# Kernel tuning notes

Measured on AMD Instinct MI355X. Metric: run time of the kernel, lower is better.

Reference implementation:

```python
import jax, jax.numpy as jnp
import numpy as np

EPS = 1e-5

def layer_norm(x, g, b):
    mu = jnp.mean(x, axis=-1, keepdims=True)
    var = jnp.var(x, axis=-1, keepdims=True)
    return (x - mu) * jax.lax.rsqrt(var + EPS) * g + b

def rel_shift(x):
    # x: [N, H, T1, T2] with T2 = 2*T1 - 1 -> [N, H, T1, T1]
    N, H, T1, T2 = x.shape
    zp = jnp.zeros((N, H, T1, 1), dtype=x.dtype)
    xp = jnp.concatenate([zp, x], axis=-1).reshape(N, H, T2 + 1, T1)
    x = xp[:, :, 1:, :].reshape(N, H, T1, T2)
    return x[:, :, :, : T2 // 2 + 1]

def setup_inputs() -> dict:
    B, T, D, Hh = 8, 1024, 512, 8
    dk = D // Hh
    P = 2 * T - 1
    key = jax.random.key(0)
    ks = jax.random.split(key, 12)
    s = 0.02
    return {
        "q": jax.random.normal(ks[0], (B, T, D), jnp.float32),
        "k": jax.random.normal(ks[1], (B, T, D), jnp.float32),
        "v": jax.random.normal(ks[2], (B, T, D), jnp.float32),
        "pos_emb": jax.random.normal(ks[3], (1, P, D), jnp.float32),
        "mask": jnp.ones((B, T, T), jnp.int32),
        "ln_q_g": jnp.ones((D,), jnp.float32), "ln_q_b": jnp.zeros((D,), jnp.float32),
        "ln_k_g": jnp.ones((D,), jnp.float32), "ln_k_b": jnp.zeros((D,), jnp.float32),
        "ln_v_g": jnp.ones((D,), jnp.float32), "ln_v_b": jnp.zeros((D,), jnp.float32),
        "w_q": jax.random.normal(ks[4], (D, D), jnp.float32) * s,   # [out, in]
        "w_k": jax.random.normal(ks[5], (D, D), jnp.float32) * s,
        "w_v": jax.random.normal(ks[6], (D, D), jnp.float32) * s,
        "w_pos": jax.random.normal(ks[7], (D, D), jnp.float32) * s,
        "w_fc": jax.random.normal(ks[8], (D, D), jnp.float32) * s,
        "pos_bias_u": jax.random.normal(ks[9], (Hh, dk), jnp.float32) * s,
        "pos_bias_v": jax.random.normal(ks[10], (Hh, dk), jnp.float32) * s,
    }

def reference(q, k, v, pos_emb, mask, ln_q_g, ln_q_b, ln_k_g, ln_k_b, ln_v_g, ln_v_b,
              w_q, w_k, w_v, w_pos, w_fc, pos_bias_u, pos_bias_v):
    B, T, D = q.shape
    H, dk = pos_bias_u.shape
    scale = 1.0 / np.sqrt(dk).astype(np.float32)
    residual = q
    qn = layer_norm(q, ln_q_g, ln_q_b)
    kn = layer_norm(k, ln_k_g, ln_k_b)
    vn = layer_norm(v, ln_v_g, ln_v_b)
    # projections (torch Linear: x @ W^T), reshape to [B, H, T, dk]
    qh = (qn @ w_q.T).reshape(B, T, H, dk)                      # [B, T, H, dk]
    kh = (kn @ w_k.T).reshape(B, T, H, dk).transpose(0, 2, 1, 3)  # [B, H, T, dk]
    vh = (vn @ w_v.T).reshape(B, T, H, dk).transpose(0, 2, 1, 3)
    p = (pos_emb @ w_pos.T).reshape(pos_emb.shape[0], -1, H, dk).transpose(0, 2, 1, 3)  # [1, H, P, dk]
    q_u = (qh + pos_bias_u).transpose(0, 2, 1, 3)  # [B, H, T, dk]
    q_v = (qh + pos_bias_v).transpose(0, 2, 1, 3)
    matrix_ac = jnp.einsum('bhqd,bhkd->bhqk', q_u, kh)          # [B, H, T, T]
    matrix_bd = jnp.einsum('bhqd,nhpd->bhqp', q_v, p)           # [B, H, T, 2T-1]
    matrix_bd = rel_shift(matrix_bd)                             # [B, H, T, T]
    scores = (matrix_ac + matrix_bd) * scale
    m = (mask[:, None, :, :] == 0)                               # [B, 1, T, T]
    scores = jnp.where(m, -jnp.inf, scores)
    attn = jax.nn.softmax(scores, axis=-1)
    attn = jnp.where(m, 0.0, attn)
    out = jnp.einsum('bhqk,bhkd->bhqd', attn, vh)                # [B, H, T, dk]
    out = out.transpose(0, 2, 1, 3).reshape(B, T, H * dk)
    out = out @ w_fc.T + residual
    return out, attn
```

## Files before the change

### kernel.cpp

```cpp
#include <hip/hip_runtime.h>

constexpr int cT  = 1024;
constexpr int cD  = 512;
constexpr int cDK = 64;
constexpr int cP  = 2047;
constexpr int PBS = 1040;

typedef __attribute__((ext_vector_type(8))) short short8;
typedef __attribute__((ext_vector_type(4))) float floatx4;

#define MFMA16(a,b,c) __builtin_amdgcn_mfma_f32_16x16x32_bf16((a),(b),(c),0,0,0)
#define SWZ(i,j) ((j) ^ ((((i) >> 2) & 3) << 3))

__device__ __forceinline__ void bar_lds(){
  asm volatile("s_waitcnt lgkmcnt(0)\n\ts_barrier" ::: "memory");
}

__device__ __forceinline__ unsigned short f2bf(float f){
  union { float f; unsigned int u; } x; x.f = f;
  unsigned int r = x.u + 0x7fffu + ((x.u >> 16) & 1u);
  return (unsigned short)(r >> 16);
}
__device__ __forceinline__ float bf2f(unsigned short h){
  union { unsigned int u; float f; } x; x.u = ((unsigned int)h) << 16;
  return x.f;
}
__device__ __forceinline__ short8 ld8(const unsigned short* p){
  return *(const short8*)p;
}

struct LN3 { const float* x[3]; const float* g[3]; const float* b[3]; unsigned short* y[3]; };
__global__ void __launch_bounds__(256) ln3_kernel(LN3 a)
{
  __shared__ float red[8];
  const int z = blockIdx.y, r = blockIdx.x;
  const float* x = a.x[z]; const float* g = a.g[z]; const float* b = a.b[z];
  unsigned short* y = a.y[z];
  const float2 v = ((const float2*)(x + (size_t)r * cD))[threadIdx.x];
  float s = v.x + v.y, sq = v.x * v.x + v.y * v.y;
  #pragma unroll
  for (int o = 32; o; o >>= 1){ s += __shfl_xor(s, o); sq += __shfl_xor(sq, o); }
  const int w = threadIdx.x >> 6;
  if ((threadIdx.x & 63) == 0){ red[w * 2] = s; red[w * 2 + 1] = sq; }
  __syncthreads();
  s  = red[0] + red[2] + red[4] + red[6];
  sq = red[1] + red[3] + red[5] + red[7];
  const float mu  = s * (1.0f / cD);
  const float var = sq * (1.0f / cD) - mu * mu;
  const float rs  = rsqrtf(var + 1e-5f);
  const int c = threadIdx.x * 2;
  const unsigned int o0 = f2bf((v.x - mu) * rs * g[c]     + b[c]);
  const unsigned int o1 = f2bf((v.y - mu) * rs * g[c + 1] + b[c + 1]);
  ((unsigned int*)(y + (size_t)r * cD))[threadIdx.x] = o0 | (o1 << 16);
}

struct Ptr5 { const float* p[5]; };
__global__ void __launch_bounds__(256) cast5_kernel(Ptr5 s, unsigned short* __restrict__ d){
  const int idx = blockIdx.x * 256 + threadIdx.x;
  const int seg = idx >> 18, off = idx & 262143;
  d[idx] = f2bf(s.p[seg][off]);
}
__global__ void __launch_bounds__(256) cast1_kernel(const float* __restrict__ s,
    unsigned short* __restrict__ d, int n){
  const int idx = blockIdx.x * 256 + threadIdx.x;
  if (idx < n) d[idx] = f2bf(s[idx]);
}

__global__ void __launch_bounds__(256) maskbits_kernel(
    const int* __restrict__ mask, unsigned int* __restrict__ bm)
{
  const int row = blockIdx.x * 4 + (threadIdx.x >> 6);
  const int lane = threadIdx.x & 63;
  #pragma unroll
  for (int ii = 0; ii < 16; ii++){
    const int m = mask[(size_t)row * cT + ii * 64 + lane];
    const unsigned long long bal = __ballot(m != 0);
    if (lane == 0)       bm[row * 32 + ii * 2]     = (unsigned int)bal;
    else if (lane == 32) bm[row * 32 + ii * 2 + 1] = (unsigned int)(bal >> 32);
  }
}

__global__ void __launch_bounds__(256, 4) gemm512_kernel(
    const unsigned short* __restrict__ A0, const unsigned short* __restrict__ W0,
    int M, int mode, float scaleA, unsigned short* __restrict__ outb,
    float* __restrict__ outf, const float* __restrict__ residual)
{
  const int z = blockIdx.z;
  const unsigned short* A = A0 + (size_t)z * 4194304;
  const unsigned short* W = W0 + (size_t)z * 262144;
  unsigned short* outz = outb ? outb + (size_t)z * 4194304 : outb;
  const float sA = (z == 0) ? scaleA : 1.0f;
  const int n0 = blockIdx.x * 128, m0 = blockIdx.y * 128;
  const int wave = threadIdx.x >> 6, lane = threadIdx.x & 63;
  const int wr = wave >> 1, wc = wave & 1;
  const int l15 = lane & 15, lq = lane >> 4;
  const int mb = m0 + wr * 64, nb = n0 + wc * 64;
  floatx4 acc[4][4];
  #pragma unroll
  for (int i = 0; i < 4; i++)
    #pragma unroll
    for (int j = 0; j < 4; j++) acc[i][j] = (floatx4){0.f, 0.f, 0.f, 0.f};
  #pragma unroll 2
  for (int k0 = 0; k0 < 512; k0 += 32){
    short8 af[4], bf[4];
    #pragma unroll
    for (int i = 0; i < 4; i++){
      int row = mb + i * 16 + l15; if (row >= M) row = M - 1;
      af[i] = ld8(A + (size_t)row * 512 + k0 + lq * 8);
      const int col = nb + i * 16 + l15;
      bf[i] = ld8(W + (size_t)col * 512 + k0 + lq * 8);
    }
    #pragma unroll
    for (int i = 0; i < 4; i++)
      #pragma unroll
      for (int j = 0; j < 4; j++)
        acc[i][j] = MFMA16(af[i], bf[j], acc[i][j]);
  }
  #pragma unroll
  for (int i = 0; i < 4; i++){
    #pragma unroll
    for (int j = 0; j < 4; j++){
      #pragma unroll
      for (int r = 0; r < 4; r++){
        const int row = mb + i * 16 + lq * 4 + r;
        const int col = nb + j * 16 + l15;
        if (row >= M) continue;
        const float val = acc[i][j][r] * sA;
        if (mode == 0){
          const int bb = row >> 10, t = row & 1023, h = col >> 6, d = col & 63;
          outz[(((size_t)(bb * 8 + h) * 1024 + t) << 6) + d] = f2bf(val);
        } else if (mode == 1){
          const int h = col >> 6, d = col & 63;
          outz[(((size_t)h * 2047 + row) << 6) + d] = f2bf(val);
        } else {
          const size_t idx = (size_t)row * 512 + col;
          outf[idx] = val + residual[idx];
        }
      }
    }
  }
}

__global__ void __launch_bounds__(256) transpose_v_kernel(
    const unsigned short* __restrict__ vh, unsigned short* __restrict__ vt)
{
  __shared__ unsigned short tile[64][65];
  const int bh = blockIdx.x, t0 = blockIdx.y * 64;
  const unsigned short* src = vh + ((size_t)bh * cT + t0) * cDK;
  #pragma unroll
  for (int i = 0; i < 16; i++){
    const int idx = threadIdx.x + i * 256;
    tile[idx >> 6][idx & 63] = src[idx];
  }
  __syncthreads();
  unsigned short* dst = vt + (size_t)bh * cDK * cT + t0;
  #pragma unroll
  for (int i = 0; i < 16; i++){
    const int idx = threadIdx.x + i * 256;
    const int d = idx >> 6, t = idx & 63;
    dst[(size_t)d * cT + t] = tile[t][d];
  }
}

__global__ void __launch_bounds__(256) dot_bias_kernel(
    const unsigned short* __restrict__ X, const float* __restrict__ bias,
    float* __restrict__ out, int rows, int hdiv, float scale)
{
  const int row = blockIdx.x * 4 + (threadIdx.x >> 6);
  const int lane = threadIdx.x & 63;
  if (row >= rows) return;
  const int h = (row / hdiv) & 7;
  float s = bf2f(X[(size_t)row * 64 + lane]) * bias[h * 64 + lane];
  #pragma unroll
  for (int o = 32; o; o >>= 1) s += __shfl_xor(s, o);
  if (lane == 0) out[row] = s * scale;
}

__global__ void __launch_bounds__(512, 4) attn_kernel(
    const unsigned short* __restrict__ qh, const unsigned short* __restrict__ kh,
    const unsigned short* __restrict__ vt, const unsigned short* __restrict__ pproj,
    const float* __restrict__ ubias, const float* __restrict__ vbias,
    const unsigned int* __restrict__ bm, float* __restrict__ attn_out,
    unsigned short* __restrict__ out_h)
{
  __shared__ float sc[16 * cT];
  unsigned short* pbuf = (unsigned short*)sc;
  const int bh = blockIdx.x, b = bh >> 3, h = bh & 7;
  const int q0 = blockIdx.y * 16;
  const int wave = threadIdx.x >> 6, lane = threadIdx.x & 63;
  const int l15 = lane & 15, lq = lane >> 4;
  const unsigned short* Q  = qh + (size_t)bh * cT * cDK;
  const unsigned short* Kp = kh + (size_t)bh * cT * cDK;
  const unsigned short* Pt = pproj + (size_t)h * cP * cDK;
  const float* ub = ubias + (size_t)bh * cT;
  const float* vb = vbias + (size_t)h * cP;

  const short8 qf0 = ld8(Q + (size_t)(q0 + l15) * cDK + lq * 8);
  const short8 qf1 = ld8(Q + (size_t)(q0 + l15) * cDK + 32 + lq * 8);

  #pragma unroll
  for (int t = 0; t < 8; t++){
    const int jt = wave + t * 8;
    const short8 kf0 = ld8(Kp + (size_t)(jt * 16 + l15) * cDK + lq * 8);
    const short8 kf1 = ld8(Kp + (size_t)(jt * 16 + l15) * cDK + 32 + lq * 8);
    floatx4 acc = (floatx4){0.f, 0.f, 0.f, 0.f};
    acc = MFMA16(qf0, kf0, acc);
    acc = MFMA16(qf1, kf1, acc);
    const int jb = jt * 16 + l15;
    const float ubv = ub[jb];
    #pragma unroll
    for (int r = 0; r < 4; r++){
      const int i = lq * 4 + r;
      sc[i * cT + (jb ^ (lq << 3))] = acc[r] + ubv + vb[jb + (cT - 1) - (q0 + i)];
    }
  }
  bar_lds();

  const int w0 = (cT - 1) - q0 - 15;
  #pragma unroll
  for (int t = 0; t < 8; t++){
    const int ct = wave + t * 8;
    const int c = ct * 16 + l15;
    int prow = w0 + c; if (prow > cP - 1) prow = cP - 1;
    const short8 pf0 = ld8(Pt + (size_t)prow * cDK + lq * 8);
    const short8 pf1 = ld8(Pt + (size_t)prow * cDK + 32 + lq * 8);
    floatx4 acc = (floatx4){0.f, 0.f, 0.f, 0.f};
    acc = MFMA16(qf0, pf0, acc);
    acc = MFMA16(qf1, pf1, acc);
    #pragma unroll
    for (int r = 0; r < 4; r++){
      const int i = lq * 4 + r;
      const int j = c - 15 + i;
      if (j >= 0 && j < cT) sc[i * cT + SWZ(i, j)] += acc[r];
    }
  }
  if (wave == 0){
    const int c = 1024 + l15;
    int prow = w0 + c; if (prow > cP - 1) prow = cP - 1;
    const short8 pf0 = ld8(Pt + (size_t)prow * cDK + lq * 8);
    const short8 pf1 = ld8(Pt + (size_t)prow * cDK + 32 + lq * 8);
    floatx4 acc = (floatx4){0.f, 0.f, 0.f, 0.f};
    acc = MFMA16(qf0, pf0, acc);
    acc = MFMA16(qf1, pf1, acc);
    #pragma unroll
    for (int r = 0; r < 4; r++){
      const int i = lq * 4 + r;
      const int j = c - 15 + i;
      if (j >= 0 && j < cT) sc[i * cT + SWZ(i, j)] += acc[r];
    }
  }
  bar_lds();

  const unsigned short* V = vt + (size_t)bh * cDK * cT;
  const int d0 = (wave & 3) * 16;
  const int kh2 = wave >> 2;
  short8 vfr[8];
  #pragma unroll
  for (int ks = 0; ks < 8; ks++){
    const int j0v = (kh2 * 16 + ks) * 32;
    vfr[ks] = ld8(V + (size_t)(d0 + l15) * cT + j0v + lq * 8);
  }

  for (int p = 0; p < 2; p++){
    const int i = p * 8 + wave;
    const int qrow = q0 + i;
    const unsigned int* bmr = bm + ((size_t)b * cT + qrow) * 32;
    const int xr = ((i >> 2) & 3) << 3;
    float vals[16];
    float mx = -INFINITY;
    #pragma unroll
    for (int ii = 0; ii < 4; ii++){
      const int j0 = lane * 4 + ii * 256;
      const unsigned int mw = bmr[(lane >> 3) + ii * 8] >> (4 * (lane & 7));
      const floatx4 sv = *(const floatx4*)&sc[i * cT + (j0 ^ xr)];
      #pragma unroll
      for (int tt = 0; tt < 4; tt++){
        float s = sv[tt];
        if (((mw >> tt) & 1u) == 0u) s = -INFINITY;
        vals[ii * 4 + tt] = s;
        mx = fmaxf(mx, s);
      }
    }
    #pragma unroll
    for (int o = 32; o; o >>= 1) mx = fmaxf(mx, __shfl_xor(mx, o));
    float sum = 0.f;
    #pragma unroll
    for (int ii = 0; ii < 16; ii++){
      const float e = (vals[ii] == -INFINITY) ? 0.f : __expf(vals[ii] - mx);
      vals[ii] = e; sum += e;
    }
    #pragma unroll
    for (int o = 32; o; o >>= 1) sum += __shfl_xor(sum, o);
    const float ri = sum > 0.f ? 1.f / sum : 0.f;
    bar_lds();
    float* arow = attn_out + ((size_t)bh * cT + qrow) * cT;
    unsigned short* prow_lds = pbuf + (size_t)i * PBS;
    #pragma unroll
    for (int ii = 0; ii < 4; ii++){
      const int j0 = lane * 4 + ii * 256;
      floatx4 pv;
      #pragma unroll
      for (int tt = 0; tt < 4; tt++) pv[tt] = vals[ii * 4 + tt] * ri;
      __builtin_nontemporal_store(pv, (floatx4*)(arow + j0));
      const unsigned int wlo = (unsigned int)f2bf(pv[0]) | ((unsigned int)f2bf(pv[1]) << 16);
      const unsigned int whi = (unsigned int)f2bf(pv[2]) | ((unsigned int)f2bf(pv[3]) << 16);
      *(unsigned long long*)(prow_lds + j0) =
          (unsigned long long)wlo | ((unsigned long long)whi << 32);
    }
  }
  bar_lds();

  floatx4 acc = (floatx4){0.f, 0.f, 0.f, 0.f};
  #pragma unroll
  for (int ks = 0; ks < 8; ks++){
    const int j0 = (kh2 * 16 + ks) * 32;
    const short8 af = ld8(pbuf + l15 * PBS + j0 + lq * 8);
    acc = MFMA16(af, vfr[ks], acc);
  }
  #pragma unroll
  for (int ks = 8; ks < 16; ks++){
    const int j0 = (kh2 * 16 + ks) * 32;
    const short8 vf = ld8(V + (size_t)(d0 + l15) * cT + j0 + lq * 8);
    const short8 af = ld8(pbuf + l15 * PBS + j0 + lq * 8);
    acc = MFMA16(af, vf, acc);
  }
  float* red4 = sc + 10240;
  if (kh2 == 1) *(floatx4*)(red4 + ((wave & 3) * 256 + lane * 4)) = acc;
  bar_lds();
  if (kh2 == 0){
    acc += *(const floatx4*)(red4 + ((wave & 3) * 256 + lane * 4));
    #pragma unroll
    for (int r = 0; r < 4; r++){
      const int i = lq * 4 + r;
      out_h[((size_t)b * cT + q0 + i) * cD + h * cDK + d0 + l15] = f2bf(acc[r]);
    }
  }
}

extern "C" void kernel_launch(void* const* d_in, const int* in_sizes, int n_in,
                              void* d_out, int out_size, void* d_ws, size_t ws_size,
                              hipStream_t stream)
{
  const float* q    = (const float*)d_in[0];
  const float* k    = (const float*)d_in[1];
  const float* v    = (const float*)d_in[2];
  const float* pe   = (const float*)d_in[3];
  const int*   mask = (const int*)d_in[4];
  const float* lnqg = (const float*)d_in[5];
  const float* lnqb = (const float*)d_in[6];
  const float* lnkg = (const float*)d_in[7];
  const float* lnkb = (const float*)d_in[8];
  const float* lnvg = (const float*)d_in[9];
  const float* lnvb = (const float*)d_in[10];
  const float* wq   = (const float*)d_in[11];
  const float* wk   = (const float*)d_in[12];
  const float* wv   = (const float*)d_in[13];
  const float* wpos = (const float*)d_in[14];
  const float* wfc  = (const float*)d_in[15];
  const float* pbu  = (const float*)d_in[16];
  const float* pbv  = (const float*)d_in[17];

  float* out_f  = (float*)d_out;
  float* attn_f = out_f + (size_t)8 * 1024 * 512;

  unsigned char* scr = (unsigned char*)attn_f;
  size_t soff = 0;
  auto salloc = [&](size_t bytes){ void* p = scr + soff; soff += (bytes + 255) & ~(size_t)255; return p; };
  unsigned short* qn   = (unsigned short*)salloc((size_t)8192 * 512 * 2);
  unsigned short* kn   = (unsigned short*)salloc((size_t)8192 * 512 * 2);
  unsigned short* vn   = (unsigned short*)salloc((size_t)8192 * 512 * 2);
  unsigned short* pe_b = (unsigned short*)salloc((size_t)2047 * 512 * 2);
  (void)kn; (void)vn;

  unsigned char* ws = (unsigned char*)d_ws;
  size_t off = 0;
  auto alloc = [&](size_t bytes){ void* p = ws + off; off += (bytes + 255) & ~(size_t)255; return p; };
  unsigned short* w5_b = (unsigned short*)alloc(5 * 512 * 512 * 2);
  unsigned short* qhb  = (unsigned short*)alloc((size_t)8192 * 512 * 2);
  unsigned short* khb  = (unsigned short*)alloc((size_t)8192 * 512 * 2);
  unsigned short* vhb  = (unsigned short*)alloc((size_t)8192 * 512 * 2);
  unsigned short* vtb  = (unsigned short*)alloc((size_t)8192 * 512 * 2);
  unsigned short* ppb  = (unsigned short*)alloc((size_t)8 * 2047 * 64 * 2);
  float*          ub   = (float*)alloc((size_t)8 * 8 * 1024 * 4);
  float*          vbias= (float*)alloc((size_t)8 * 2047 * 4);
  unsigned short* ohb  = (unsigned short*)alloc((size_t)8192 * 512 * 2);
  unsigned int*   bmask= (unsigned int*)alloc((size_t)8192 * 32 * 4);
  (void)ws_size; (void)n_in; (void)in_sizes; (void)out_size;

  Ptr5 c5; c5.p[0] = wq; c5.p[1] = wk; c5.p[2] = wv; c5.p[3] = wpos; c5.p[4] = wfc;
  cast5_kernel<<<5120, 256, 0, stream>>>(c5, w5_b);
  cast1_kernel<<<4094, 256, 0, stream>>>(pe, pe_b, 2047 * 512);
  maskbits_kernel<<<2048, 256, 0, stream>>>(mask, bmask);

  LN3 l3;
  l3.x[0] = q; l3.x[1] = k; l3.x[2] = v;
  l3.g[0] = lnqg; l3.g[1] = lnkg; l3.g[2] = lnvg;
  l3.b[0] = lnqb; l3.b[1] = lnkb; l3.b[2] = lnvb;
  l3.y[0] = qn; l3.y[1] = kn; l3.y[2] = vn;
  ln3_kernel<<<dim3(8192, 3), 256, 0, stream>>>(l3);

  gemm512_kernel<<<dim3(4, 64, 3), 256, 0, stream>>>(qn, w5_b, 8192, 0, 0.125f,
                                                     qhb, nullptr, nullptr);
  gemm512_kernel<<<dim3(4, 16, 1), 256, 0, stream>>>(pe_b, w5_b + 3 * 262144, 2047, 1, 1.0f,
                                                     ppb, nullptr, nullptr);

  transpose_v_kernel<<<dim3(64, 16), 256, 0, stream>>>(vhb, vtb);

  dot_bias_kernel<<<16384, 256, 0, stream>>>(khb, pbu, ub, 65536, 1024, 0.125f);
  dot_bias_kernel<<<4094, 256, 0, stream>>>(ppb, pbv, vbias, 16376, 2047, 0.125f);

  attn_kernel<<<dim3(64, 64), 512, 0, stream>>>(qhb, khb, vtb, ppb, ub, vbias,
                                                bmask, attn_f, ohb);

  gemm512_kernel<<<dim3(4, 64, 1), 256, 0, stream>>>(ohb, w5_b + 4 * 262144, 8192, 2, 1.0f,
                                                     nullptr, out_f, q);
}
```

Measured before the change: 686.5 us.

## Fold pos_bias_u into Q projection, drop ub kernel, prefetch K/P/V fragments

The u-bias term is folded into the Q projection epilogue by adding pos_bias_u to q before scaling. The v-bias dot product then uses (pos_bias_v - pos_bias_u), which removes the per-key ub dot_bias kernel, its buffer, and its per-element reads inside attention. The attention kernel also batches its K and P fragment loads ahead of the MFMAs, hoists the vbias reads, and prefetches the second half of the V fragments before the second softmax pass. The LayerNorm kernel now handles two rows per block with float4 loads. The extra register arrays raise register pressure, which can reduce occupancy of the attention kernel.

```diff
diff --git a/kernel.cpp b/kernel.cpp
--- a/kernel.cpp
+++ b/kernel.cpp
@@ -33,25 +33,33 @@
 __global__ void __launch_bounds__(256) ln3_kernel(LN3 a)
 {
   __shared__ float red[8];
-  const int z = blockIdx.y, r = blockIdx.x;
+  const int z = blockIdx.y;
+  const int half = threadIdx.x >> 7;
+  const int r = blockIdx.x * 2 + half;
+  const int tid = threadIdx.x & 127;
   const float* x = a.x[z]; const float* g = a.g[z]; const float* b = a.b[z];
   unsigned short* y = a.y[z];
-  const float2 v = ((const float2*)(x + (size_t)r * cD))[threadIdx.x];
-  float s = v.x + v.y, sq = v.x * v.x + v.y * v.y;
+  const float4 v = ((const float4*)(x + (size_t)r * cD))[tid];
+  float s  = v.x + v.y + v.z + v.w;
+  float sq = v.x * v.x + v.y * v.y + v.z * v.z + v.w * v.w;
   #pragma unroll
   for (int o = 32; o; o >>= 1){ s += __shfl_xor(s, o); sq += __shfl_xor(sq, o); }
-  const int w = threadIdx.x >> 6;
-  if ((threadIdx.x & 63) == 0){ red[w * 2] = s; red[w * 2 + 1] = sq; }
+  const int w = (threadIdx.x >> 6) & 1;
+  if ((threadIdx.x & 63) == 0){ red[half * 4 + w * 2] = s; red[half * 4 + w * 2 + 1] = sq; }
   __syncthreads();
-  s  = red[0] + red[2] + red[4] + red[6];
-  sq = red[1] + red[3] + red[5] + red[7];
+  s  = red[half * 4]     + red[half * 4 + 2];
+  sq = red[half * 4 + 1] + red[half * 4 + 3];
   const float mu  = s * (1.0f / cD);
   const float var = sq * (1.0f / cD) - mu * mu;
   const float rs  = rsqrtf(var + 1e-5f);
-  const int c = threadIdx.x * 2;
-  const unsigned int o0 = f2bf((v.x - mu) * rs * g[c]     + b[c]);
-  const unsigned int o1 = f2bf((v.y - mu) * rs * g[c + 1] + b[c + 1]);
-  ((unsigned int*)(y + (size_t)r * cD))[threadIdx.x] = o0 | (o1 << 16);
+  const int c = tid * 4;
+  const float4 gv = *(const float4*)(g + c);
+  const float4 bv = *(const float4*)(b + c);
+  const unsigned int o0 = (unsigned int)f2bf((v.x - mu) * rs * gv.x + bv.x)
+                        | ((unsigned int)f2bf((v.y - mu) * rs * gv.y + bv.y) << 16);
+  const unsigned int o1 = (unsigned int)f2bf((v.z - mu) * rs * gv.z + bv.z)
+                        | ((unsigned int)f2bf((v.w - mu) * rs * gv.w + bv.w) << 16);
+  ((uint2*)(y + (size_t)r * cD))[tid] = make_uint2(o0, o1);
 }
 
 struct Ptr5 { const float* p[5]; };
@@ -83,7 +91,8 @@
 __global__ void __launch_bounds__(256, 4) gemm512_kernel(
     const unsigned short* __restrict__ A0, const unsigned short* __restrict__ W0,
     int M, int mode, float scaleA, unsigned short* __restrict__ outb,
-    float* __restrict__ outf, const float* __restrict__ residual)
+    float* __restrict__ outf, const float* __restrict__ residual,
+    const float* __restrict__ addq)
 {
   const int z = blockIdx.z;
   const unsigned short* A = A0 + (size_t)z * 4194304;
@@ -125,7 +134,9 @@
         const int row = mb + i * 16 + lq * 4 + r;
         const int col = nb + j * 16 + l15;
         if (row >= M) continue;
-        const float val = acc[i][j][r] * sA;
+        float val = acc[i][j][r];
+        if (mode == 0 && z == 0 && addq) val += addq[col];
+        val *= sA;
         if (mode == 0){
           const int bb = row >> 10, t = row & 1023, h = col >> 6, d = col & 63;
           outz[(((size_t)(bb * 8 + h) * 1024 + t) << 6) + d] = f2bf(val);
@@ -164,13 +175,16 @@
 
 __global__ void __launch_bounds__(256) dot_bias_kernel(
     const unsigned short* __restrict__ X, const float* __restrict__ bias,
-    float* __restrict__ out, int rows, int hdiv, float scale)
+    const float* __restrict__ bias2, float* __restrict__ out,
+    int rows, int hdiv, float scale)
 {
   const int row = blockIdx.x * 4 + (threadIdx.x >> 6);
   const int lane = threadIdx.x & 63;
   if (row >= rows) return;
   const int h = (row / hdiv) & 7;
-  float s = bf2f(X[(size_t)row * 64 + lane]) * bias[h * 64 + lane];
+  float bv = bias[h * 64 + lane];
+  if (bias2) bv -= bias2[h * 64 + lane];
+  float s = bf2f(X[(size_t)row * 64 + lane]) * bv;
   #pragma unroll
   for (int o = 32; o; o >>= 1) s += __shfl_xor(s, o);
   if (lane == 0) out[row] = s * scale;
@@ -179,9 +193,8 @@
 __global__ void __launch_bounds__(512, 4) attn_kernel(
     const unsigned short* __restrict__ qh, const unsigned short* __restrict__ kh,
     const unsigned short* __restrict__ vt, const unsigned short* __restrict__ pproj,
-    const float* __restrict__ ubias, const float* __restrict__ vbias,
-    const unsigned int* __restrict__ bm, float* __restrict__ attn_out,
-    unsigned short* __restrict__ out_h)
+    const float* __restrict__ vbias, const unsigned int* __restrict__ bm,
+    float* __restrict__ attn_out, unsigned short* __restrict__ out_h)
 {
   __shared__ float sc[16 * cT];
   unsigned short* pbuf = (unsigned short*)sc;
@@ -192,46 +205,59 @@
   const unsigned short* Q  = qh + (size_t)bh * cT * cDK;
   const unsigned short* Kp = kh + (size_t)bh * cT * cDK;
   const unsigned short* Pt = pproj + (size_t)h * cP * cDK;
-  const float* ub = ubias + (size_t)bh * cT;
   const float* vb = vbias + (size_t)h * cP;
 
   const short8 qf0 = ld8(Q + (size_t)(q0 + l15) * cDK + lq * 8);
   const short8 qf1 = ld8(Q + (size_t)(q0 + l15) * cDK + 32 + lq * 8);
 
-  #pragma unroll
-  for (int t = 0; t < 8; t++){
-    const int jt = wave + t * 8;
-    const short8 kf0 = ld8(Kp + (size_t)(jt * 16 + l15) * cDK + lq * 8);
-    const short8 kf1 = ld8(Kp + (size_t)(jt * 16 + l15) * cDK + 32 + lq * 8);
-    floatx4 acc = (floatx4){0.f, 0.f, 0.f, 0.f};
-    acc = MFMA16(qf0, kf0, acc);
-    acc = MFMA16(qf1, kf1, acc);
-    const int jb = jt * 16 + l15;
-    const float ubv = ub[jb];
-    #pragma unroll
-    for (int r = 0; r < 4; r++){
-      const int i = lq * 4 + r;
-      sc[i * cT + (jb ^ (lq << 3))] = acc[r] + ubv + vb[jb + (cT - 1) - (q0 + i)];
+  {
+    short8 k0a[8], k1a[8];
+    #pragma unroll
+    for (int t = 0; t < 8; t++){
+      const int jt = wave + t * 8;
+      k0a[t] = ld8(Kp + (size_t)(jt * 16 + l15) * cDK + lq * 8);
+      k1a[t] = ld8(Kp + (size_t)(jt * 16 + l15) * cDK + 32 + lq * 8);
+    }
+    #pragma unroll
+    for (int t = 0; t < 8; t++){
+      const int jt = wave + t * 8;
+      floatx4 acc = (floatx4){0.f, 0.f, 0.f, 0.f};
+      acc = MFMA16(qf0, k0a[t], acc);
+      acc = MFMA16(qf1, k1a[t], acc);
+      const int jb = jt * 16 + l15;
+      #pragma unroll
+      for (int r = 0; r < 4; r++){
+        const int i = lq * 4 + r;
+        sc[i * cT + (jb ^ (lq << 3))] = acc[r];
+      }
     }
   }
   bar_lds();
 
   const int w0 = (cT - 1) - q0 - 15;
-  #pragma unroll
-  for (int t = 0; t < 8; t++){
-    const int ct = wave + t * 8;
-    const int c = ct * 16 + l15;
-    int prow = w0 + c; if (prow > cP - 1) prow = cP - 1;
-    const short8 pf0 = ld8(Pt + (size_t)prow * cDK + lq * 8);
-    const short8 pf1 = ld8(Pt + (size_t)prow * cDK + 32 + lq * 8);
-    floatx4 acc = (floatx4){0.f, 0.f, 0.f, 0.f};
-    acc = MFMA16(qf0, pf0, acc);
-    acc = MFMA16(qf1, pf1, acc);
-    #pragma unroll
-    for (int r = 0; r < 4; r++){
-      const int i = lq * 4 + r;
-      const int j = c - 15 + i;
-      if (j >= 0 && j < cT) sc[i * cT + SWZ(i, j)] += acc[r];
+  {
+    short8 p0a[8], p1a[8];
+    float vba[8];
+    #pragma unroll
+    for (int t = 0; t < 8; t++){
+      const int c = (wave + t * 8) * 16 + l15;
+      int prow = w0 + c; if (prow > cP - 1) prow = cP - 1;
+      p0a[t] = ld8(Pt + (size_t)prow * cDK + lq * 8);
+      p1a[t] = ld8(Pt + (size_t)prow * cDK + 32 + lq * 8);
+      vba[t] = vb[prow];
+    }
+    #pragma unroll
+    for (int t = 0; t < 8; t++){
+      const int c = (wave + t * 8) * 16 + l15;
+      floatx4 acc = (floatx4){0.f, 0.f, 0.f, 0.f};
+      acc = MFMA16(qf0, p0a[t], acc);
+      acc = MFMA16(qf1, p1a[t], acc);
+      #pragma unroll
+      for (int r = 0; r < 4; r++){
+        const int i = lq * 4 + r;
+        const int j = c - 15 + i;
+        if (j >= 0 && j < cT) sc[i * cT + SWZ(i, j)] += acc[r] + vba[t];
+      }
     }
   }
   if (wave == 0){
@@ -239,6 +265,7 @@
     int prow = w0 + c; if (prow > cP - 1) prow = cP - 1;
     const short8 pf0 = ld8(Pt + (size_t)prow * cDK + lq * 8);
     const short8 pf1 = ld8(Pt + (size_t)prow * cDK + 32 + lq * 8);
+    const float vbv = vb[prow];
     floatx4 acc = (floatx4){0.f, 0.f, 0.f, 0.f};
     acc = MFMA16(qf0, pf0, acc);
     acc = MFMA16(qf1, pf1, acc);
@@ -246,7 +273,7 @@
     for (int r = 0; r < 4; r++){
       const int i = lq * 4 + r;
       const int j = c - 15 + i;
-      if (j >= 0 && j < cT) sc[i * cT + SWZ(i, j)] += acc[r];
+      if (j >= 0 && j < cT) sc[i * cT + SWZ(i, j)] += acc[r] + vbv;
     }
   }
   bar_lds();
@@ -254,14 +281,22 @@
   const unsigned short* V = vt + (size_t)bh * cDK * cT;
   const int d0 = (wave & 3) * 16;
   const int kh2 = wave >> 2;
-  short8 vfr[8];
+  short8 vfr[8], vfb[8];
   #pragma unroll
   for (int ks = 0; ks < 8; ks++){
     const int j0v = (kh2 * 16 + ks) * 32;
     vfr[ks] = ld8(V + (size_t)(d0 + l15) * cT + j0v + lq * 8);
   }
 
+  #pragma unroll
   for (int p = 0; p < 2; p++){
+    if (p == 1){
+      #pragma unroll
+      for (int ks = 0; ks < 8; ks++){
+        const int j0v = (kh2 * 16 + ks + 8) * 32;
+        vfb[ks] = ld8(V + (size_t)(d0 + l15) * cT + j0v + lq * 8);
+      }
+    }
     const int i = p * 8 + wave;
     const int qrow = q0 + i;
     const unsigned int* bmr = bm + ((size_t)b * cT + qrow) * 32;
@@ -320,9 +355,8 @@
   #pragma unroll
   for (int ks = 8; ks < 16; ks++){
     const int j0 = (kh2 * 16 + ks) * 32;
-    const short8 vf = ld8(V + (size_t)(d0 + l15) * cT + j0 + lq * 8);
     const short8 af = ld8(pbuf + l15 * PBS + j0 + lq * 8);
-    acc = MFMA16(af, vf, acc);
+    acc = MFMA16(af, vfb[ks - 8], acc);
   }
   float* red4 = sc + 10240;
   if (kh2 == 1) *(floatx4*)(red4 + ((wave & 3) * 256 + lane * 4)) = acc;
@@ -381,7 +415,6 @@
   unsigned short* vhb  = (unsigned short*)alloc((size_t)8192 * 512 * 2);
   unsigned short* vtb  = (unsigned short*)alloc((size_t)8192 * 512 * 2);
   unsigned short* ppb  = (unsigned short*)alloc((size_t)8 * 2047 * 64 * 2);
-  float*          ub   = (float*)alloc((size_t)8 * 8 * 1024 * 4);
   float*          vbias= (float*)alloc((size_t)8 * 2047 * 4);
   unsigned short* ohb  = (unsigned short*)alloc((size_t)8192 * 512 * 2);
   unsigned int*   bmask= (unsigned int*)alloc((size_t)8192 * 32 * 4);
@@ -397,21 +430,20 @@
   l3.g[0] = lnqg; l3.g[1] = lnkg; l3.g[2] = lnvg;
   l3.b[0] = lnqb; l3.b[1] = lnkb; l3.b[2] = lnvb;
   l3.y[0] = qn; l3.y[1] = kn; l3.y[2] = vn;
-  ln3_kernel<<<dim3(8192, 3), 256, 0, stream>>>(l3);
+  ln3_kernel<<<dim3(4096, 3), 256, 0, stream>>>(l3);
 
   gemm512_kernel<<<dim3(4, 64, 3), 256, 0, stream>>>(qn, w5_b, 8192, 0, 0.125f,
-                                                     qhb, nullptr, nullptr);
+                                                     qhb, nullptr, nullptr, pbu);
   gemm512_kernel<<<dim3(4, 16, 1), 256, 0, stream>>>(pe_b, w5_b + 3 * 262144, 2047, 1, 1.0f,
-                                                     ppb, nullptr, nullptr);
+                                                     ppb, nullptr, nullptr, nullptr);
 
   transpose_v_kernel<<<dim3(64, 16), 256, 0, stream>>>(vhb, vtb);
 
-  dot_bias_kernel<<<16384, 256, 0, stream>>>(khb, pbu, ub, 65536, 1024, 0.125f);
-  dot_bias_kernel<<<4094, 256, 0, stream>>>(ppb, pbv, vbias, 16376, 2047, 0.125f);
-
-  attn_kernel<<<dim3(64, 64), 512, 0, stream>>>(qhb, khb, vtb, ppb, ub, vbias,
+  dot_bias_kernel<<<4094, 256, 0, stream>>>(ppb, pbv, pbu, vbias, 16376, 2047, 0.125f);
+
+  attn_kernel<<<dim3(64, 64), 512, 0, stream>>>(qhb, khb, vtb, ppb, vbias,
                                                 bmask, attn_f, ohb);
 
   gemm512_kernel<<<dim3(4, 64, 1), 256, 0, stream>>>(ohb, w5_b + 4 * 262144, 8192, 2, 1.0f,
-                                                     nullptr, out_f, q);
-}
+                                                     nullptr, out_f, q, nullptr);
+}
```

Result: faster. 671.5 us (-2.2%).
